# Optimization experiments

Measured on AMD Instinct MI355X. Metric: run time of the kernel, lower is better.

Reference implementation:

```python
import jax, jax.numpy as jnp
import numpy as np

B, C, H, W = 8, 64, 64, 64  # module requires c == h == w due to view/permute quirk


def setup_inputs() -> dict:
    key = jax.random.key(0)
    ks = jax.random.split(key, 5)
    return {
        "x": jax.random.normal(ks[0], (B, C, H, W), dtype=jnp.float32),
        "w_qkv": jax.random.normal(ks[1], (3 * C, C), dtype=jnp.float32) * (1.0 / np.sqrt(C)),
        "b_qkv": jax.random.normal(ks[2], (3 * C,), dtype=jnp.float32) * 0.02,
        "w_out": jax.random.normal(ks[3], (C, C), dtype=jnp.float32) * (1.0 / np.sqrt(C)),
        "b_out": jax.random.normal(ks[4], (C,), dtype=jnp.float32) * 0.02,
    }


def reference(x, w_qkv, b_qkv, w_out, b_out):
    b, c, h, w = x.shape
    # 1x1 conv == channel matmul (norm='none' -> Identity, the only runnable branch)
    qkv = jnp.einsum('bchw,oc->bohw', x, w_qkv) + b_qkv[None, :, None, None]
    q, k, v = jnp.split(qkv, 3, axis=1)  # each (b, c, h, w)

    def flat(t):  # (b,c,h,w) -> (b, h*w, c), matches permute(0,2,3,1).view
        return t.transpose(0, 2, 3, 1).reshape(b, h * w, c)

    q, k, v = flat(q), flat(k), flat(v)
    scale = 1.0 / jnp.sqrt(jnp.asarray(c, dtype=x.dtype))
    scores = jax.nn.softmax(jnp.einsum('bqc,bkc->bqk', q, k) * scale, axis=-1)
    out = jnp.einsum('bqk,bkc->bqc', scores, v)  # (b, hw, c)
    # Faithfully replicate the original's view(b,c,h,w).permute(0,3,1,2) quirk
    out = out.reshape(b, c, h, w).transpose(0, 3, 1, 2)  # (b, w, c, h); needs c==h==w
    out = jnp.einsum('bchw,oc->bohw', out, w_out) + b_out[None, :, None, None]
    return out + x
```

## Files before the change

kernel.cpp:

```cpp
#include <hip/hip_runtime.h>
#include <hip/hip_bf16.h>
#include <stdint.h>

typedef unsigned short u16;
typedef __attribute__((ext_vector_type(8))) short bf16x8;
typedef __attribute__((ext_vector_type(4))) float f32x4;
typedef __attribute__((ext_vector_type(2))) float f32x2;
typedef __attribute__((ext_vector_type(4))) unsigned int u32x4;
typedef __attribute__((ext_vector_type(2))) unsigned int u32x2;

#define NTOK 4096
#define NT32 32

#if __has_builtin(__builtin_amdgcn_exp2f)
#define EXP2F __builtin_amdgcn_exp2f
#else
#define EXP2F exp2f
#endif

__device__ __forceinline__ f32x4 MFMA(bf16x8 a, bf16x8 b, f32x4 c) {
    return __builtin_amdgcn_mfma_f32_16x16x32_bf16(a, b, c, 0, 0, 0);
}

__device__ __forceinline__ uint32_t pk_bf16(float a, float b) {
    uint32_t d;
    asm("v_cvt_pk_bf16_f32 %0, %1, %2" : "=v"(d) : "v"(a), "v"(b));
    return d;
}

__device__ __forceinline__ void hilo_pack8(const float* v, bf16x8* h, bf16x8* l) {
    union { uint32_t u[4]; bf16x8 b; } H, L;
#pragma unroll
    for (int m = 0; m < 4; ++m) {
        const uint32_t ua = __float_as_uint(v[2*m]);
        const uint32_t ub = __float_as_uint(v[2*m+1]);
        const float la = v[2*m]   - __uint_as_float(ua & 0xffff0000u);
        const float lb = v[2*m+1] - __uint_as_float(ub & 0xffff0000u);
        H.u[m] = (ua >> 16) | (ub & 0xffff0000u);
        L.u[m] = (__float_as_uint(la) >> 16) | (__float_as_uint(lb) & 0xffff0000u);
    }
    *h = H.b; *l = L.b;
}

__global__ __launch_bounds__(256) void k_qkv(
    const float* __restrict__ x, const float* __restrict__ wqkv, const float* __restrict__ bqkv,
    u16* __restrict__ Qp, u16* __restrict__ Kp, u16* __restrict__ Vp)
{
    __shared__ float qt_lds[64 * 194];
    const int blk = blockIdx.x;
    const int b   = blk >> 6;
    const int tb  = (blk & 63) << 6;
    const int tid = threadIdx.x;
    const int lane = tid & 63;
    const int wv  = __builtin_amdgcn_readfirstlane(tid >> 6);
    const int r   = lane & 15;
    const int g   = lane >> 4;
    const int o0  = wv * 48;

    bf16x8 wh[3][2], wl[3][2];
#pragma unroll
    for (int oi = 0; oi < 3; ++oi)
#pragma unroll
        for (int ks = 0; ks < 2; ++ks) {
            const float* wp = wqkv + (size_t)(o0 + oi*16 + r) * 64 + ks*32 + g*8;
            float wv8[8];
            *(f32x4*)(wv8)     = *(const f32x4*)(wp);
            *(f32x4*)(wv8 + 4) = *(const f32x4*)(wp + 4);
            hilo_pack8(wv8, &wh[oi][ks], &wl[oi][ks]);
        }

    f32x4 acc[3][4];
#pragma unroll
    for (int oi = 0; oi < 3; ++oi)
#pragma unroll
        for (int tt = 0; tt < 4; ++tt) acc[oi][tt] = 0.f;

#pragma unroll
    for (int tt = 0; tt < 4; ++tt) {
        bf16x8 xh[2], xl[2];
#pragma unroll
        for (int ks = 0; ks < 2; ++ks) {
            float xv[8];
#pragma unroll
            for (int j = 0; j < 8; ++j)
                xv[j] = x[(size_t)(b*64 + ks*32 + g*8 + j) * NTOK + tb + tt*16 + r];
            hilo_pack8(xv, &xh[ks], &xl[ks]);
        }
#pragma unroll
        for (int oi = 0; oi < 3; ++oi) {
            f32x4 a = acc[oi][tt];
            a = MFMA(wh[oi][0], xh[0], a);
            a = MFMA(wh[oi][1], xh[1], a);
            a = MFMA(wl[oi][0], xh[0], a);
            a = MFMA(wl[oi][1], xh[1], a);
            a = MFMA(wh[oi][0], xl[0], a);
            a = MFMA(wh[oi][1], xl[1], a);
            acc[oi][tt] = a;
        }
    }

#pragma unroll
    for (int oi = 0; oi < 3; ++oi)
#pragma unroll
        for (int tt = 0; tt < 4; ++tt)
#pragma unroll
            for (int i = 0; i < 4; ++i)
                qt_lds[(tt*16 + r) * 194 + o0 + oi*16 + g*4 + i] = acc[oi][tt][i];
    __syncthreads();

    const float SC = 0.18033688011112042f;

    {
        const int t = tid >> 2, c0 = (tid & 3) * 16;
        float v[16], bq[16];
#pragma unroll
        for (int m = 0; m < 8; ++m)
            *(f32x2*)(v + 2*m) = *(const f32x2*)&qt_lds[t*194 + c0 + 2*m];
#pragma unroll
        for (int m = 0; m < 4; ++m)
            *(f32x4*)(bq + 4*m) = *(const f32x4*)(bqkv + c0 + 4*m);
        u32x4 P0, P1;
#pragma unroll
        for (int m = 0; m < 4; ++m) {
            P0[m] = pk_bf16((v[2*m]   + bq[2*m]  ) * SC, (v[2*m+1] + bq[2*m+1]) * SC);
            P1[m] = pk_bf16((v[8+2*m] + bq[8+2*m]) * SC, (v[9+2*m] + bq[9+2*m]) * SC);
        }
        size_t base = ((size_t)(b * NTOK + tb + t)) * 64 + c0;
        *(u32x4*)(Qp + base)     = P0;
        *(u32x4*)(Qp + base + 8) = P1;
    }

#pragma unroll
    for (int uu = 0; uu < 2; ++uu) {
        const int u  = tid * 2 + uu;
        const int t  = u >> 3;
        const int ks = (u >> 2) & 1;
        const int gk = u & 3;
        const int cb0 = 64 + ks*32 + gk*8;
        float v[8];
#pragma unroll
        for (int m = 0; m < 4; ++m)
            *(f32x2*)(v + 2*m) = *(const f32x2*)&qt_lds[t*194 + cb0 + 2*m];
        u32x4 P;
#pragma unroll
        for (int m = 0; m < 4; ++m)
            P[m] = pk_bf16(v[2*m] + bqkv[cb0 + 2*m], v[2*m+1] + bqkv[cb0 + 2*m+1]);
        const int tg = tb + t;
        size_t kbase = (size_t)b * 262144 + ((size_t)(tg >> 4) * 2 + ks) * 512 + gk*128 + (t & 15) * 8;
        *(u32x4*)(Kp + kbase) = P;
    }

    {
        const int cb = (tid >> 4) & 3;
        const int r2 = tid & 15;
        const float bv = bqkv[128 + cb*16 + r2];
        const int T = (blk & 63) >> 1;
        const int halfb = blk & 1;
#pragma unroll
        for (int m = 0; m < 4; ++m) {
            const int tq = m * 4 + (tid >> 6);
            float v[4];
#pragma unroll
            for (int jj = 0; jj < 4; ++jj)
                v[jj] = qt_lds[(tq*4 + jj)*194 + 128 + cb*16 + r2] + bv;
            const int t = tq * 4;
            const int wtr = halfb*2 + (t >> 5);
            const int sti = (t >> 4) & 1;
            const int g2  = (t >> 2) & 3;
            u32x2 W;
            W[0] = pk_bf16(v[0], v[1]);
            W[1] = pk_bf16(v[2], v[3]);
            size_t vbase = (size_t)b * 262144 +
                           (((size_t)T * 4 + wtr) * 4 + cb) * 512 + (g2*16 + r2) * 8 + sti * 4;
            *(u32x2*)(Vp + vbase) = W;
        }
    }
}

__global__ __launch_bounds__(256, 2) void k_attn(
    const u16* __restrict__ Qp, const u16* __restrict__ Kp, const u16* __restrict__ Vp,
    const float* __restrict__ wout, const float* __restrict__ bout,
    const float* __restrict__ x, float* __restrict__ out)
{
    __shared__ float larr[4][64];
    __shared__ float otbuf[2][64 * 67];
    const int hw  = blockIdx.x;
    const int b   = hw & 7;
    const int qt  = hw >> 3;
    const int tid = threadIdx.x;
    const int lane = tid & 63;
    const int wt2 = tid >> 6;
    const int r   = lane & 15;
    const int g   = lane >> 4;
    const int row0 = qt * 64;

    bf16x8 qh[4][2];
#pragma unroll
    for (int rt = 0; rt < 4; ++rt) {
        const size_t qoff = ((size_t)(b * NTOK + row0 + rt*16 + r)) * 64 + g * 8;
        qh[rt][0] = *(const bf16x8*)(Qp + qoff);
        qh[rt][1] = *(const bf16x8*)(Qp + qoff + 32);
    }

    const u16* kbase = Kp + (size_t)b * 262144 + wt2 * 2048 + (size_t)lane * 8;
    const u16* vptr  = Vp + (size_t)b * 262144 + wt2 * 2048 + (size_t)lane * 8;

    bf16x8 ONES;
#pragma unroll
    for (int j = 0; j < 8; ++j) ONES[j] = (short)0x3F80;

    f32x4 oacc[4][4];
#pragma unroll
    for (int rt = 0; rt < 4; ++rt)
#pragma unroll
        for (int cb = 0; cb < 4; ++cb) oacc[rt][cb] = 0.f;
    f32x4 lacc[4];
#pragma unroll
    for (int rt = 0; rt < 4; ++rt) lacc[rt] = 0.f;

    bf16x8 kA[2][2], kB[2][2];
#pragma unroll
    for (int sti = 0; sti < 2; ++sti)
#pragma unroll
        for (int ks = 0; ks < 2; ++ks) {
            kA[sti][ks] = *(const bf16x8*)(kbase + 0*8192 + sti*1024 + ks*512);
            kB[sti][ks] = *(const bf16x8*)(kbase + 1*8192 + sti*1024 + ks*512);
        }

    auto halfrt = [&](bf16x8 (&kb)[2][2], bf16x8 (&vf)[4], int rt0) {
        f32x4 s[2][2];
        __builtin_amdgcn_s_setprio(1);
#pragma unroll
        for (int rr = 0; rr < 2; ++rr)
#pragma unroll
            for (int sti = 0; sti < 2; ++sti) {
                f32x4 a = {0.f, 0.f, 0.f, 0.f};
                a = MFMA(kb[sti][0], qh[rt0 + rr][0], a);
                a = MFMA(kb[sti][1], qh[rt0 + rr][1], a);
                s[rr][sti] = a;
            }
        __builtin_amdgcn_s_setprio(0);

#pragma unroll
        for (int rr = 0; rr < 2; ++rr) {
            const int rt = rt0 + rr;
            float p[8];
#pragma unroll
            for (int sti = 0; sti < 2; ++sti)
#pragma unroll
                for (int i = 0; i < 4; ++i)
                    p[sti*4 + i] = EXP2F(s[rr][sti][i]);
            union { uint32_t u[4]; bf16x8 b; } PA;
#pragma unroll
            for (int m = 0; m < 4; ++m) PA.u[m] = pk_bf16(p[2*m], p[2*m+1]);
            __builtin_amdgcn_s_setprio(1);
#pragma unroll
            for (int cb = 0; cb < 4; ++cb)
                oacc[rt][cb] = MFMA(PA.b, vf[cb], oacc[rt][cb]);
            lacc[rt] = MFMA(PA.b, ONES, lacc[rt]);
            __builtin_amdgcn_s_setprio(0);
        }
    };

    auto body = [&](bf16x8 (&kb)[2][2], int Tp) {
        bf16x8 vf[4];
#pragma unroll
        for (int cb = 0; cb < 4; ++cb)
            vf[cb] = *(const bf16x8*)(vptr + cb*512);
        vptr += 8192;

        halfrt(kb, vf, 0);
        halfrt(kb, vf, 2);

        const u16* kp = kbase + (size_t)Tp * 8192;
#pragma unroll
        for (int sti = 0; sti < 2; ++sti)
#pragma unroll
            for (int ks = 0; ks < 2; ++ks)
                kb[sti][ks] = *(const bf16x8*)(kp + sti*1024 + ks*512);
    };

    for (int T = 0; T < NT32; T += 2) {
        const int TpA = (T + 2 < NT32) ? T + 2 : NT32 - 1;
        const int TpB = (T + 3 < NT32) ? T + 3 : NT32 - 1;
        body(kA, TpA);
        body(kB, TpB);
    }

    if (r == 0) {
#pragma unroll
        for (int rt = 0; rt < 4; ++rt)
#pragma unroll
            for (int i = 0; i < 4; ++i)
                larr[wt2][rt*16 + g*4 + i] = lacc[rt][i];
    }

    if (wt2 < 2) {
        float* ob = otbuf[wt2];
#pragma unroll
        for (int rt = 0; rt < 4; ++rt)
#pragma unroll
            for (int cb = 0; cb < 4; ++cb)
#pragma unroll
                for (int i = 0; i < 4; ++i)
                    ob[(rt*16 + g*4 + i)*67 + cb*16 + r] = oacc[rt][cb][i];
    }
    __syncthreads();
    if (wt2 >= 2) {
        float* ob = otbuf[wt2 - 2];
#pragma unroll
        for (int rt = 0; rt < 4; ++rt)
#pragma unroll
            for (int cb = 0; cb < 4; ++cb)
#pragma unroll
                for (int i = 0; i < 4; ++i)
                    ob[(rt*16 + g*4 + i)*67 + cb*16 + r] += oacc[rt][cb][i];
    }
    __syncthreads();

    const int orow = wt2*16 + r;
    const float inv = 1.0f / (larr[0][orow] + larr[1][orow] + larr[2][orow] + larr[3][orow]);
    bf16x8 oh_[2], ol_[2];
#pragma unroll
    for (int ks = 0; ks < 2; ++ks) {
        float ov[8];
#pragma unroll
        for (int j = 0; j < 8; ++j) {
            const int idx = orow*67 + ks*32 + g*8 + j;
            ov[j] = (otbuf[0][idx] + otbuf[1][idx]) * inv;
        }
        hilo_pack8(ov, &oh_[ks], &ol_[ks]);
    }
#pragma unroll
    for (int ot = 0; ot < 4; ++ot) {
        bf16x8 wh2[2], wl2[2];
#pragma unroll
        for (int ks = 0; ks < 2; ++ks) {
            const float* wp = wout + (size_t)(ot*16 + r) * 64 + ks*32 + g*8;
            float wv8[8];
            *(f32x4*)(wv8)     = *(const f32x4*)(wp);
            *(f32x4*)(wv8 + 4) = *(const f32x4*)(wp + 4);
            hilo_pack8(wv8, &wh2[ks], &wl2[ks]);
        }
        f32x4 a = {0.f, 0.f, 0.f, 0.f};
        a = MFMA(wh2[0], oh_[0], a);
        a = MFMA(wh2[1], oh_[1], a);
        a = MFMA(wl2[0], oh_[0], a);
        a = MFMA(wl2[1], oh_[1], a);
        a = MFMA(wh2[0], ol_[0], a);
        a = MFMA(wh2[1], ol_[1], a);
#pragma unroll
        for (int i = 0; i < 4; ++i) {
            const int oo = ot*16 + g*4 + i;
            const size_t xi = ((size_t)(b*64 + oo)) * NTOK + row0 + wt2*16 + r;
            out[xi] = a[i] + bout[oo] + x[xi];
        }
    }
}

extern "C" void kernel_launch(void* const* d_in, const int* in_sizes, int n_in,
                              void* d_out, int out_size, void* d_ws, size_t ws_size,
                              hipStream_t stream)
{
    (void)in_sizes; (void)n_in; (void)out_size; (void)ws_size;
    const float* x    = (const float*)d_in[0];
    const float* wqkv = (const float*)d_in[1];
    const float* bqkv = (const float*)d_in[2];
    const float* wout = (const float*)d_in[3];
    const float* bout = (const float*)d_in[4];
    float* out = (float*)d_out;

    char* ws = (char*)d_ws;
    const size_t MB = 1024 * 1024;
    u16* Qp = (u16*)(ws);
    u16* Kp = (u16*)(ws + 4 * MB);
    u16* Vp = (u16*)(ws + 8 * MB);

    k_qkv<<<512, 256, 0, stream>>>(x, wqkv, bqkv, Qp, Kp, Vp);
    k_attn<<<512, 256, 0, stream>>>(Qp, Kp, Vp, wout, bout, x, out);
}
```

Baseline: 53.97 us.

## Split attention over key halves into partial outputs with separate epilogue kernel

Splits the key/value sequence into two halves so the attention kernel launches 1024 blocks, each writing unnormalized fp32 partial outputs and row sums to workspace. A new k_out kernel combines the two partials, normalizes, and applies the output projection, bias and residual. It also replaces the ones-vector MFMA for row sums with scalar adds plus shuffles, drops the double-buffered K prefetch, and raises launch bounds to 3 blocks per SM. The intent is more parallelism and occupancy, at the cost of an extra launch and about 16 MB of partial-result traffic.

```diff
diff --git a/kernel.cpp b/kernel.cpp
--- a/kernel.cpp
+++ b/kernel.cpp
@@ -10,7 +10,7 @@
 typedef __attribute__((ext_vector_type(2))) unsigned int u32x2;
 
 #define NTOK 4096
-#define NT32 32
+#define NTHALF 16
 
 #if __has_builtin(__builtin_amdgcn_exp2f)
 #define EXP2F __builtin_amdgcn_exp2f
@@ -177,13 +177,150 @@
     }
 }
 
-__global__ __launch_bounds__(256, 2) void k_attn(
+__global__ __launch_bounds__(256, 3) void k_attn(
     const u16* __restrict__ Qp, const u16* __restrict__ Kp, const u16* __restrict__ Vp,
+    float* __restrict__ Opart, float* __restrict__ Lpart)
+{
+    __shared__ float otbuf[2][64 * 68];
+    __shared__ float larr[4][64];
+    const int hw  = blockIdx.x;
+    const int b   = hw & 7;
+    const int rest = hw >> 3;
+    const int qt  = rest >> 1;
+    const int kh  = rest & 1;
+    const int tid = threadIdx.x;
+    const int lane = tid & 63;
+    const int wt2 = tid >> 6;
+    const int r   = lane & 15;
+    const int g   = lane >> 4;
+    const int row0 = qt * 64;
+
+    bf16x8 qh[4][2];
+#pragma unroll
+    for (int rt = 0; rt < 4; ++rt) {
+        const size_t qoff = ((size_t)(b * NTOK + row0 + rt*16 + r)) * 64 + g * 8;
+        qh[rt][0] = *(const bf16x8*)(Qp + qoff);
+        qh[rt][1] = *(const bf16x8*)(Qp + qoff + 32);
+    }
+
+    const u16* kptr = Kp + (size_t)b * 262144 + (size_t)kh * NTHALF * 8192 + wt2 * 2048 + (size_t)lane * 8;
+    const u16* vptr = Vp + (size_t)b * 262144 + (size_t)kh * NTHALF * 8192 + wt2 * 2048 + (size_t)lane * 8;
+
+    f32x4 oacc[4][4];
+#pragma unroll
+    for (int rt = 0; rt < 4; ++rt)
+#pragma unroll
+        for (int cb = 0; cb < 4; ++cb) oacc[rt][cb] = 0.f;
+    float lpart[4] = {0.f, 0.f, 0.f, 0.f};
+
+    for (int T = 0; T < NTHALF; ++T) {
+        bf16x8 kc[2][2];
+#pragma unroll
+        for (int sti = 0; sti < 2; ++sti)
+#pragma unroll
+            for (int ks = 0; ks < 2; ++ks)
+                kc[sti][ks] = *(const bf16x8*)(kptr + sti*1024 + ks*512);
+        bf16x8 vf[4];
+#pragma unroll
+        for (int cb = 0; cb < 4; ++cb)
+            vf[cb] = *(const bf16x8*)(vptr + cb*512);
+        kptr += 8192;
+        vptr += 8192;
+
+#pragma unroll
+        for (int rp = 0; rp < 2; ++rp) {
+            f32x4 s[2][2];
+            __builtin_amdgcn_s_setprio(1);
+#pragma unroll
+            for (int rr = 0; rr < 2; ++rr)
+#pragma unroll
+                for (int sti = 0; sti < 2; ++sti) {
+                    f32x4 a = {0.f, 0.f, 0.f, 0.f};
+                    a = MFMA(kc[sti][0], qh[rp*2 + rr][0], a);
+                    a = MFMA(kc[sti][1], qh[rp*2 + rr][1], a);
+                    s[rr][sti] = a;
+                }
+            __builtin_amdgcn_s_setprio(0);
+
+#pragma unroll
+            for (int rr = 0; rr < 2; ++rr) {
+                const int rt = rp*2 + rr;
+                float p[8];
+#pragma unroll
+                for (int sti = 0; sti < 2; ++sti)
+#pragma unroll
+                    for (int i = 0; i < 4; ++i)
+                        p[sti*4 + i] = EXP2F(s[rr][sti][i]);
+                lpart[rt] += ((p[0]+p[1]) + (p[2]+p[3])) + ((p[4]+p[5]) + (p[6]+p[7]));
+                union { uint32_t u[4]; bf16x8 b; } PA;
+#pragma unroll
+                for (int m = 0; m < 4; ++m) PA.u[m] = pk_bf16(p[2*m], p[2*m+1]);
+                __builtin_amdgcn_s_setprio(1);
+#pragma unroll
+                for (int cb = 0; cb < 4; ++cb)
+                    oacc[rt][cb] = MFMA(PA.b, vf[cb], oacc[rt][cb]);
+                __builtin_amdgcn_s_setprio(0);
+            }
+        }
+    }
+
+#pragma unroll
+    for (int rt = 0; rt < 4; ++rt) {
+        float v = lpart[rt];
+        v += __shfl_xor(v, 16);
+        v += __shfl_xor(v, 32);
+        lpart[rt] = v;
+    }
+    if (lane < 16) {
+#pragma unroll
+        for (int rt = 0; rt < 4; ++rt)
+            larr[wt2][rt*16 + lane] = lpart[rt];
+    }
+
+    if (wt2 < 2) {
+        float* ob = otbuf[wt2];
+#pragma unroll
+        for (int rt = 0; rt < 4; ++rt)
+#pragma unroll
+            for (int cb = 0; cb < 4; ++cb)
+#pragma unroll
+                for (int i = 0; i < 4; ++i)
+                    ob[(rt*16 + g*4 + i)*68 + cb*16 + r] = oacc[rt][cb][i];
+    }
+    __syncthreads();
+    if (wt2 >= 2) {
+        float* ob = otbuf[wt2 - 2];
+#pragma unroll
+        for (int rt = 0; rt < 4; ++rt)
+#pragma unroll
+            for (int cb = 0; cb < 4; ++cb)
+#pragma unroll
+                for (int i = 0; i < 4; ++i)
+                    ob[(rt*16 + g*4 + i)*68 + cb*16 + r] += oacc[rt][cb][i];
+    }
+    __syncthreads();
+
+    float* OB = Opart + (((size_t)(b * 64 + qt)) * 2 + kh) * 4096;
+    {
+        const int row = tid >> 2, c0 = (tid & 3) * 16;
+#pragma unroll
+        for (int m = 0; m < 4; ++m) {
+            f32x4 v0 = *(const f32x4*)&otbuf[0][row*68 + c0 + 4*m];
+            f32x4 v1 = *(const f32x4*)&otbuf[1][row*68 + c0 + 4*m];
+            *(f32x4*)&OB[row*64 + c0 + 4*m] = v0 + v1;
+        }
+    }
+    if (tid < 64) {
+        Lpart[(((size_t)(b * 64 + qt)) * 2 + kh) * 64 + tid] =
+            larr[0][tid] + larr[1][tid] + larr[2][tid] + larr[3][tid];
+    }
+}
+
+__global__ __launch_bounds__(256) void k_out(
+    const float* __restrict__ Opart, const float* __restrict__ Lpart,
     const float* __restrict__ wout, const float* __restrict__ bout,
     const float* __restrict__ x, float* __restrict__ out)
 {
-    __shared__ float larr[4][64];
-    __shared__ float otbuf[2][64 * 67];
     const int hw  = blockIdx.x;
     const int b   = hw & 7;
     const int qt  = hw >> 3;
@@ -194,140 +331,25 @@
     const int g   = lane >> 4;
     const int row0 = qt * 64;
 
-    bf16x8 qh[4][2];
-#pragma unroll
-    for (int rt = 0; rt < 4; ++rt) {
-        const size_t qoff = ((size_t)(b * NTOK + row0 + rt*16 + r)) * 64 + g * 8;
-        qh[rt][0] = *(const bf16x8*)(Qp + qoff);
-        qh[rt][1] = *(const bf16x8*)(Qp + qoff + 32);
-    }
-
-    const u16* kbase = Kp + (size_t)b * 262144 + wt2 * 2048 + (size_t)lane * 8;
-    const u16* vptr  = Vp + (size_t)b * 262144 + wt2 * 2048 + (size_t)lane * 8;
-
-    bf16x8 ONES;
-#pragma unroll
-    for (int j = 0; j < 8; ++j) ONES[j] = (short)0x3F80;
-
-    f32x4 oacc[4][4];
-#pragma unroll
-    for (int rt = 0; rt < 4; ++rt)
-#pragma unroll
-        for (int cb = 0; cb < 4; ++cb) oacc[rt][cb] = 0.f;
-    f32x4 lacc[4];
-#pragma unroll
-    for (int rt = 0; rt < 4; ++rt) lacc[rt] = 0.f;
-
-    bf16x8 kA[2][2], kB[2][2];
-#pragma unroll
-    for (int sti = 0; sti < 2; ++sti)
-#pragma unroll
-        for (int ks = 0; ks < 2; ++ks) {
-            kA[sti][ks] = *(const bf16x8*)(kbase + 0*8192 + sti*1024 + ks*512);
-            kB[sti][ks] = *(const bf16x8*)(kbase + 1*8192 + sti*1024 + ks*512);
-        }
-
-    auto halfrt = [&](bf16x8 (&kb)[2][2], bf16x8 (&vf)[4], int rt0) {
-        f32x4 s[2][2];
-        __builtin_amdgcn_s_setprio(1);
-#pragma unroll
-        for (int rr = 0; rr < 2; ++rr)
-#pragma unroll
-            for (int sti = 0; sti < 2; ++sti) {
-                f32x4 a = {0.f, 0.f, 0.f, 0.f};
-                a = MFMA(kb[sti][0], qh[rt0 + rr][0], a);
-                a = MFMA(kb[sti][1], qh[rt0 + rr][1], a);
-                s[rr][sti] = a;
-            }
-        __builtin_amdgcn_s_setprio(0);
-
-#pragma unroll
-        for (int rr = 0; rr < 2; ++rr) {
-            const int rt = rt0 + rr;
-            float p[8];
-#pragma unroll
-            for (int sti = 0; sti < 2; ++sti)
-#pragma unroll
-                for (int i = 0; i < 4; ++i)
-                    p[sti*4 + i] = EXP2F(s[rr][sti][i]);
-            union { uint32_t u[4]; bf16x8 b; } PA;
-#pragma unroll
-            for (int m = 0; m < 4; ++m) PA.u[m] = pk_bf16(p[2*m], p[2*m+1]);
-            __builtin_amdgcn_s_setprio(1);
-#pragma unroll
-            for (int cb = 0; cb < 4; ++cb)
-                oacc[rt][cb] = MFMA(PA.b, vf[cb], oacc[rt][cb]);
-            lacc[rt] = MFMA(PA.b, ONES, lacc[rt]);
-            __builtin_amdgcn_s_setprio(0);
-        }
-    };
-
-    auto body = [&](bf16x8 (&kb)[2][2], int Tp) {
-        bf16x8 vf[4];
-#pragma unroll
-        for (int cb = 0; cb < 4; ++cb)
-            vf[cb] = *(const bf16x8*)(vptr + cb*512);
-        vptr += 8192;
-
-        halfrt(kb, vf, 0);
-        halfrt(kb, vf, 2);
-
-        const u16* kp = kbase + (size_t)Tp * 8192;
-#pragma unroll
-        for (int sti = 0; sti < 2; ++sti)
-#pragma unroll
-            for (int ks = 0; ks < 2; ++ks)
-                kb[sti][ks] = *(const bf16x8*)(kp + sti*1024 + ks*512);
-    };
-
-    for (int T = 0; T < NT32; T += 2) {
-        const int TpA = (T + 2 < NT32) ? T + 2 : NT32 - 1;
-        const int TpB = (T + 3 < NT32) ? T + 3 : NT32 - 1;
-        body(kA, TpA);
-        body(kB, TpB);
-    }
-
-    if (r == 0) {
-#pragma unroll
-        for (int rt = 0; rt < 4; ++rt)
-#pragma unroll
-            for (int i = 0; i < 4; ++i)
-                larr[wt2][rt*16 + g*4 + i] = lacc[rt][i];
-    }
-
-    if (wt2 < 2) {
-        float* ob = otbuf[wt2];
-#pragma unroll
-        for (int rt = 0; rt < 4; ++rt)
-#pragma unroll
-            for (int cb = 0; cb < 4; ++cb)
-#pragma unroll
-                for (int i = 0; i < 4; ++i)
-                    ob[(rt*16 + g*4 + i)*67 + cb*16 + r] = oacc[rt][cb][i];
-    }
-    __syncthreads();
-    if (wt2 >= 2) {
-        float* ob = otbuf[wt2 - 2];
-#pragma unroll
-        for (int rt = 0; rt < 4; ++rt)
-#pragma unroll
-            for (int cb = 0; cb < 4; ++cb)
-#pragma unroll
-                for (int i = 0; i < 4; ++i)
-                    ob[(rt*16 + g*4 + i)*67 + cb*16 + r] += oacc[rt][cb][i];
-    }
-    __syncthreads();
+    const float* O0 = Opart + ((size_t)(b * 64 + qt)) * 2 * 4096;
+    const float* O1 = O0 + 4096;
+    const float* L  = Lpart + ((size_t)(b * 64 + qt)) * 2 * 64;
 
     const int orow = wt2*16 + r;
-    const float inv = 1.0f / (larr[0][orow] + larr[1][orow] + larr[2][orow] + larr[3][orow]);
+    const float inv = 1.0f / (L[orow] + L[64 + orow]);
+
     bf16x8 oh_[2], ol_[2];
 #pragma unroll
     for (int ks = 0; ks < 2; ++ks) {
         float ov[8];
-#pragma unroll
-        for (int j = 0; j < 8; ++j) {
-            const int idx = orow*67 + ks*32 + g*8 + j;
-            ov[j] = (otbuf[0][idx] + otbuf[1][idx]) * inv;
+        f32x4 a0 = *(const f32x4*)&O0[orow*64 + ks*32 + g*8];
+        f32x4 a1 = *(const f32x4*)&O0[orow*64 + ks*32 + g*8 + 4];
+        f32x4 b0 = *(const f32x4*)&O1[orow*64 + ks*32 + g*8];
+        f32x4 b1 = *(const f32x4*)&O1[orow*64 + ks*32 + g*8 + 4];
+#pragma unroll
+        for (int i = 0; i < 4; ++i) {
+            ov[i]     = (a0[i] + b0[i]) * inv;
+            ov[4 + i] = (a1[i] + b1[i]) * inv;
         }
         hilo_pack8(ov, &oh_[ks], &ol_[ks]);
     }
@@ -372,10 +394,13 @@
 
     char* ws = (char*)d_ws;
     const size_t MB = 1024 * 1024;
-    u16* Qp = (u16*)(ws);
-    u16* Kp = (u16*)(ws + 4 * MB);
-    u16* Vp = (u16*)(ws + 8 * MB);
+    u16*   Qp    = (u16*)(ws);
+    u16*   Kp    = (u16*)(ws + 4 * MB);
+    u16*   Vp    = (u16*)(ws + 8 * MB);
+    float* Opart = (float*)(ws + 12 * MB);
+    float* Lpart = (float*)(ws + 29 * MB);
 
     k_qkv<<<512, 256, 0, stream>>>(x, wqkv, bqkv, Qp, Kp, Vp);
-    k_attn<<<512, 256, 0, stream>>>(Qp, Kp, Vp, wout, bout, x, out);
-}
+    k_attn<<<1024, 256, 0, stream>>>(Qp, Kp, Vp, Opart, Lpart);
+    k_out<<<512, 256, 0, stream>>>(Opart, Lpart, wout, bout, x, out);
+}
```

After: 60.73 us. 1.13x slower.
